# Performance work log

Measured on AMD Instinct MI355X. Metric: run time of the kernel, lower is better.

## Reference

```python
import jax, jax.numpy as jnp
import numpy as np

TOP_K = 4
NORM_TOPK_PROB = True


def setup_inputs() -> dict:
    key = jax.random.key(0)
    kx, kg, k1, k3, k2 = jax.random.split(key, 5)
    B, S, H, I, E = 1, 2048, 1024, 512, 16
    scale = 0.02
    return {
        "hidden_states": jax.random.normal(kx, (B, S, H), jnp.float32),
        "gate_w": jax.random.normal(kg, (E, H), jnp.float32) * scale,   # router Linear weight [E,H]
        "w1": jax.random.normal(k1, (E, I, H), jnp.float32) * scale,    # intermediateDense per expert
        "w3": jax.random.normal(k3, (E, I, H), jnp.float32) * scale,    # intermediateDense2 per expert
        "w2": jax.random.normal(k2, (E, H, I), jnp.float32) * scale,    # outputDense per expert
    }


def reference(hidden_states, gate_w, w1, w3, w2):
    B, S, H = hidden_states.shape
    x = hidden_states.reshape(-1, H)                    # [T,H]
    T = x.shape[0]
    E = gate_w.shape[0]

    # Router: softmax in fp32, top-k, optional renorm (norm_topk_prob=True)
    router_logits = x @ gate_w.T                        # [T,E]
    probs = jax.nn.softmax(router_logits.astype(jnp.float32), axis=-1)
    routing_weights, selected = jax.lax.top_k(probs, TOP_K)   # [T,K], [T,K]
    if NORM_TOPK_PROB:
        routing_weights = routing_weights / routing_weights.sum(-1, keepdims=True)
    routing_weights = routing_weights.astype(x.dtype)

    # Dense per-token expert-weight matrix: zero for unselected experts, so
    # the combine below computes exactly the torch gather->FFN->index_add math.
    w = jnp.zeros((T, E), x.dtype).at[jnp.arange(T)[:, None], selected].add(routing_weights)

    # Gated SiLU FFN for every expert, combined with routing weights.
    h1 = jnp.einsum('th,eih->tei', x, w1)               # [T,E,I]
    h3 = jnp.einsum('th,eih->tei', x, w3)               # [T,E,I]
    act = jax.nn.silu(h1) * h3                          # [T,E,I]
    out = jnp.einsum('tei,ehi,te->th', act, w2, w)      # [T,H]
    return out.reshape(B, S, H)
```

## Files before the change

### kernel.cpp

```cpp
#include <hip/hip_runtime.h>
#include <hip/hip_bf16.h>

#define T 2048
#define H 1024
#define IDIM 512
#define E 16
#define TOPK 4
#define NPAIR (T * TOPK)

typedef short bf16x8 __attribute__((ext_vector_type(8)));
typedef float f32x4 __attribute__((ext_vector_type(4)));

static __device__ __forceinline__ unsigned short f2bf(float f) {
    union { float f; unsigned int u; } v; v.f = f;
    unsigned int r = (v.u + 0x7FFFu + ((v.u >> 16) & 1u)) >> 16;
    return (unsigned short)r;
}
static __device__ __forceinline__ float bf2f(unsigned short s) {
    union { unsigned int u; float f; } v; v.u = ((unsigned int)s) << 16;
    return v.f;
}

static __device__ __forceinline__ void async_ld16(const unsigned short* g, unsigned short* l) {
    __builtin_amdgcn_global_load_lds((const __attribute__((address_space(1))) void*)g,
                                     (__attribute__((address_space(3))) void*)l, 16, 0, 0);
}

__global__ __launch_bounds__(256) void cvt_kernel(
    const float* __restrict__ src, unsigned short* __restrict__ dst, int n4)
{
    int i = blockIdx.x * blockDim.x + threadIdx.x;
    int stride = gridDim.x * blockDim.x;
    for (; i < n4; i += stride) {
        float4 v = ((const float4*)src)[i];
        ushort4 o;
        o.x = f2bf(v.x); o.y = f2bf(v.y); o.z = f2bf(v.z); o.w = f2bf(v.w);
        ((ushort4*)dst)[i] = o;
    }
}

__global__ __launch_bounds__(256) void router_kernel(
    const float* __restrict__ x, const float* __restrict__ gw,
    int* __restrict__ topk_idx, float* __restrict__ topk_w,
    unsigned short* __restrict__ xb)
{
    int tok = blockIdx.x * 4 + (threadIdx.x >> 6);
    int lane = threadIdx.x & 63;
    if (tok >= T) return;
    const float4* xt4 = (const float4*)(x + (size_t)tok * H);
    float4 xr[4];
#pragma unroll
    for (int j = 0; j < 4; ++j) xr[j] = xt4[lane + j * 64];
    ushort4* xbt = (ushort4*)(xb + (size_t)tok * H);
#pragma unroll
    for (int j = 0; j < 4; ++j) {
        ushort4 o;
        o.x = f2bf(xr[j].x); o.y = f2bf(xr[j].y);
        o.z = f2bf(xr[j].z); o.w = f2bf(xr[j].w);
        xbt[lane + j * 64] = o;
    }
    float logits[E];
#pragma unroll
    for (int e = 0; e < E; ++e) {
        const float4* ge4 = (const float4*)(gw + (size_t)e * H);
        float acc = 0.f;
#pragma unroll
        for (int j = 0; j < 4; ++j) {
            float4 g = ge4[lane + j * 64];
            acc += xr[j].x * g.x + xr[j].y * g.y + xr[j].z * g.z + xr[j].w * g.w;
        }
#pragma unroll
        for (int off = 32; off; off >>= 1) acc += __shfl_xor(acc, off, 64);
        logits[e] = acc;
    }
    if (lane == 0) {
        float m = logits[0];
#pragma unroll
        for (int e = 1; e < E; ++e) m = fmaxf(m, logits[e]);
        float p[E];
#pragma unroll
        for (int e = 0; e < E; ++e) p[e] = __expf(logits[e] - m);
        int sel[TOPK]; float wv[TOPK]; float tot = 0.f;
#pragma unroll
        for (int k = 0; k < TOPK; ++k) {
            int best = 0; float bv = -1.f;
#pragma unroll
            for (int e = 0; e < E; ++e) { if (p[e] > bv) { bv = p[e]; best = e; } }
            sel[k] = best; wv[k] = bv; tot += bv; p[best] = -2.f;
        }
#pragma unroll
        for (int k = 0; k < TOPK; ++k) {
            topk_idx[tok * TOPK + k] = sel[k];
            topk_w[tok * TOPK + k] = wv[k] / tot;
        }
    }
}

__global__ __launch_bounds__(256) void hist_kernel(
    const int* __restrict__ topk_idx, int* __restrict__ offsets)
{
    __shared__ int h[4][E];
    int tid = threadIdx.x, wave = tid >> 6;
    if (tid < 4 * E) ((int*)h)[tid] = 0;
    __syncthreads();
    for (int i = tid; i < NPAIR; i += 256) atomicAdd(&h[wave][topk_idx[i]], 1);
    __syncthreads();
    if (tid == 0) {
        int s = 0;
#pragma unroll
        for (int e = 0; e < E; ++e) {
            offsets[e] = s;
            s += h[0][e] + h[1][e] + h[2][e] + h[3][e];
        }
        offsets[E] = s;
    }
}

__global__ __launch_bounds__(256) void scatter_kernel(
    const int* __restrict__ topk_idx,
    const int* __restrict__ offsets, int* __restrict__ cursor,
    int* __restrict__ pair_token, int* __restrict__ inv_pos)
{
    __shared__ int lh[E];
    __shared__ int base[E];
    int tid = threadIdx.x;
    int i = blockIdx.x * 256 + tid;
    if (tid < E) lh[tid] = 0;
    __syncthreads();
    int e = topk_idx[i];
    int lr = atomicAdd(&lh[e], 1);
    __syncthreads();
    if (tid < E) base[tid] = atomicAdd(&cursor[tid], lh[tid]);
    __syncthreads();
    int pos = offsets[e] + base[e] + lr;
    pair_token[pos] = i >> 2;
    inv_pos[i] = pos;
}

__global__ __launch_bounds__(256) void gemm_a_kernel(
    const unsigned short* __restrict__ xb,
    const unsigned short* __restrict__ wb1,
    const unsigned short* __restrict__ wb3,
    const int* __restrict__ offsets,
    const int* __restrict__ pair_token,
    unsigned short* __restrict__ act)
{
    __shared__ unsigned short Xs[2][128 * 64];
    __shared__ unsigned short W1s[2][64 * 64];
    __shared__ unsigned short W3s[2][64 * 64];

    int bid = blockIdx.x;
    int xcd = bid & 7, s = bid >> 3;
    int yz = xcd * 16 + (s >> 4);
    int e = yz >> 3;
    int n0 = (yz & 7) * 64;
    int t0 = (s & 15) * 128;

    int beg = offsets[e];
    int cnt = offsets[e + 1] - beg;
    if (t0 >= cnt) return;

    int tid = threadIdx.x;
    int wave = tid >> 6, lane = tid & 63;
    int lrow8 = lane >> 3;
    int csw = (lane & 7) ^ lrow8;

    const unsigned short* xg[4];
#pragma unroll
    for (int i = 0; i < 4; ++i) {
        int row = wave * 32 + i * 8 + lrow8;
        int r = t0 + row; if (r >= cnt) r = cnt - 1;
        xg[i] = xb + (size_t)pair_token[beg + r] * H + csw * 8;
    }
    const unsigned short* w1g[2];
    const unsigned short* w3g[2];
    size_t wbase = (size_t)e * IDIM * H;
#pragma unroll
    for (int i = 0; i < 2; ++i) {
        int row = wave * 16 + i * 8 + lrow8;
        w1g[i] = wb1 + wbase + (size_t)(n0 + row) * H + csw * 8;
        w3g[i] = wb3 + wbase + (size_t)(n0 + row) * H + csw * 8;
    }

    int wr = wave >> 1, wc = wave & 1;
    int lm = lane & 15, lq = lane >> 4;

    f32x4 acc1[4][2], acc3[4][2];
#pragma unroll
    for (int mi = 0; mi < 4; ++mi)
#pragma unroll
        for (int nj = 0; nj < 2; ++nj) {
            acc1[mi][nj] = (f32x4){0.f, 0.f, 0.f, 0.f};
            acc3[mi][nj] = (f32x4){0.f, 0.f, 0.f, 0.f};
        }

#pragma unroll
    for (int i = 0; i < 4; ++i) async_ld16(xg[i], &Xs[0][(wave * 32 + i * 8) * 64]);
#pragma unroll
    for (int i = 0; i < 2; ++i) {
        async_ld16(w1g[i], &W1s[0][(wave * 16 + i * 8) * 64]);
        async_ld16(w3g[i], &W3s[0][(wave * 16 + i * 8) * 64]);
    }

    const int NK = H / 64;
    for (int kk = 0; kk < NK; ++kk) {
        int cur = kk & 1;
        __syncthreads();
        if (kk + 1 < NK) {
            int nxt = cur ^ 1;
            int k1 = (kk + 1) * 64;
#pragma unroll
            for (int i = 0; i < 4; ++i) async_ld16(xg[i] + k1, &Xs[nxt][(wave * 32 + i * 8) * 64]);
#pragma unroll
            for (int i = 0; i < 2; ++i) {
                async_ld16(w1g[i] + k1, &W1s[nxt][(wave * 16 + i * 8) * 64]);
                async_ld16(w3g[i] + k1, &W3s[nxt][(wave * 16 + i * 8) * 64]);
            }
        }
#pragma unroll
        for (int ks = 0; ks < 2; ++ks) {
            int cc = ks * 4 + lq;
            bf16x8 af[4], b1[2], b3[2];
#pragma unroll
            for (int mi = 0; mi < 4; ++mi) {
                int m = wr * 64 + mi * 16 + lm;
                af[mi] = *(const bf16x8*)&Xs[cur][m * 64 + ((cc ^ (m & 7)) << 3)];
            }
#pragma unroll
            for (int nj = 0; nj < 2; ++nj) {
                int n = wc * 32 + nj * 16 + lm;
                b1[nj] = *(const bf16x8*)&W1s[cur][n * 64 + ((cc ^ (n & 7)) << 3)];
                b3[nj] = *(const bf16x8*)&W3s[cur][n * 64 + ((cc ^ (n & 7)) << 3)];
            }
#pragma unroll
            for (int mi = 0; mi < 4; ++mi)
#pragma unroll
                for (int nj = 0; nj < 2; ++nj) {
                    acc1[mi][nj] = __builtin_amdgcn_mfma_f32_16x16x32_bf16(af[mi], b1[nj], acc1[mi][nj], 0, 0, 0);
                    acc3[mi][nj] = __builtin_amdgcn_mfma_f32_16x16x32_bf16(af[mi], b3[nj], acc3[mi][nj], 0, 0, 0);
                }
        }
    }
#pragma unroll
    for (int mi = 0; mi < 4; ++mi) {
#pragma unroll
        for (int r = 0; r < 4; ++r) {
            int trow = t0 + wr * 64 + mi * 16 + lq * 4 + r;
            if (trow < cnt) {
                size_t base = (size_t)(beg + trow) * IDIM + n0 + wc * 32 + lm;
#pragma unroll
                for (int nj = 0; nj < 2; ++nj) {
                    float h1 = acc1[mi][nj][r];
                    float sg = h1 / (1.f + __expf(-h1));
                    act[base + nj * 16] = f2bf(sg * acc3[mi][nj][r]);
                }
            }
        }
    }
}

__global__ __launch_bounds__(256) void gemm_b_kernel(
    const unsigned short* __restrict__ act,
    const unsigned short* __restrict__ wb2,
    const int* __restrict__ offsets,
    unsigned short* __restrict__ outp)
{
    __shared__ unsigned short As[2][128 * 64];
    __shared__ unsigned short W2s[2][64 * 64];

    int bid = blockIdx.x;
    int xcd = bid & 7, s = bid >> 3;
    int yz = xcd * 32 + (s >> 4);
    int e = yz >> 4;
    int h0 = (yz & 15) * 64;
    int t0 = (s & 15) * 128;

    int beg = offsets[e];
    int cnt = offsets[e + 1] - beg;
    if (t0 >= cnt) return;

    int tid = threadIdx.x;
    int wave = tid >> 6, lane = tid & 63;
    int lrow8 = lane >> 3;
    int csw = (lane & 7) ^ lrow8;

    const unsigned short* ag[4];
#pragma unroll
    for (int i = 0; i < 4; ++i) {
        int row = wave * 32 + i * 8 + lrow8;
        int ar = beg + t0 + row; if (ar > NPAIR - 1) ar = NPAIR - 1;
        ag[i] = act + (size_t)ar * IDIM + csw * 8;
    }
    const unsigned short* w2g[2];
    size_t wbase = (size_t)e * H * IDIM;
#pragma unroll
    for (int i = 0; i < 2; ++i) {
        int row = wave * 16 + i * 8 + lrow8;
        w2g[i] = wb2 + wbase + (size_t)(h0 + row) * IDIM + csw * 8;
    }

    int wr = wave >> 1, wc = wave & 1;
    int lm = lane & 15, lq = lane >> 4;

    f32x4 acc[4][2];
#pragma unroll
    for (int mi = 0; mi < 4; ++mi)
#pragma unroll
        for (int nj = 0; nj < 2; ++nj) acc[mi][nj] = (f32x4){0.f, 0.f, 0.f, 0.f};

#pragma unroll
    for (int i = 0; i < 4; ++i) async_ld16(ag[i], &As[0][(wave * 32 + i * 8) * 64]);
#pragma unroll
    for (int i = 0; i < 2; ++i) async_ld16(w2g[i], &W2s[0][(wave * 16 + i * 8) * 64]);

    const int NK = IDIM / 64;
    for (int kk = 0; kk < NK; ++kk) {
        int cur = kk & 1;
        __syncthreads();
        if (kk + 1 < NK) {
            int nxt = cur ^ 1;
            int k1 = (kk + 1) * 64;
#pragma unroll
            for (int i = 0; i < 4; ++i) async_ld16(ag[i] + k1, &As[nxt][(wave * 32 + i * 8) * 64]);
#pragma unroll
            for (int i = 0; i < 2; ++i) async_ld16(w2g[i] + k1, &W2s[nxt][(wave * 16 + i * 8) * 64]);
        }
#pragma unroll
        for (int ks = 0; ks < 2; ++ks) {
            int cc = ks * 4 + lq;
            bf16x8 af[4], bfr[2];
#pragma unroll
            for (int mi = 0; mi < 4; ++mi) {
                int m = wr * 64 + mi * 16 + lm;
                af[mi] = *(const bf16x8*)&As[cur][m * 64 + ((cc ^ (m & 7)) << 3)];
            }
#pragma unroll
            for (int nj = 0; nj < 2; ++nj) {
                int n = wc * 32 + nj * 16 + lm;
                bfr[nj] = *(const bf16x8*)&W2s[cur][n * 64 + ((cc ^ (n & 7)) << 3)];
            }
#pragma unroll
            for (int mi = 0; mi < 4; ++mi)
#pragma unroll
                for (int nj = 0; nj < 2; ++nj)
                    acc[mi][nj] = __builtin_amdgcn_mfma_f32_16x16x32_bf16(af[mi], bfr[nj], acc[mi][nj], 0, 0, 0);
        }
    }
#pragma unroll
    for (int mi = 0; mi < 4; ++mi) {
#pragma unroll
        for (int r = 0; r < 4; ++r) {
            int trow = t0 + wr * 64 + mi * 16 + lq * 4 + r;
            if (trow < cnt) {
                unsigned short* orow = outp + (size_t)(beg + trow) * H + h0 + wc * 32 + lm;
#pragma unroll
                for (int nj = 0; nj < 2; ++nj) orow[nj * 16] = f2bf(acc[mi][nj][r]);
            }
        }
    }
}

__global__ __launch_bounds__(256) void combine_kernel(
    const unsigned short* __restrict__ outp, const int* __restrict__ inv_pos,
    const float* __restrict__ topk_w, float* __restrict__ out)
{
    int gid = blockIdx.x * 256 + threadIdx.x;
    int t = gid >> 8;
    int c4 = gid & 255;
    float4 a = make_float4(0.f, 0.f, 0.f, 0.f);
#pragma unroll
    for (int k = 0; k < TOPK; ++k) {
        int pos = inv_pos[t * TOPK + k];
        float w = topk_w[t * TOPK + k];
        ushort4 v = ((const ushort4*)(outp + (size_t)pos * H))[c4];
        a.x += w * bf2f(v.x); a.y += w * bf2f(v.y);
        a.z += w * bf2f(v.z); a.w += w * bf2f(v.w);
    }
    *(float4*)(out + (size_t)t * H + c4 * 4) = a;
}

extern "C" void kernel_launch(void* const* d_in, const int* in_sizes, int n_in,
                              void* d_out, int out_size, void* d_ws, size_t ws_size,
                              hipStream_t stream)
{
    const float* x  = (const float*)d_in[0];
    const float* gw = (const float*)d_in[1];
    const float* w1 = (const float*)d_in[2];
    const float* w3 = (const float*)d_in[3];
    const float* w2 = (const float*)d_in[4];
    float* out = (float*)d_out;

    char* ws = (char*)d_ws;
    int*   cursor     = (int*)(ws + 64);
    int*   offsets    = (int*)(ws + 128);
    int*   topk_idx   = (int*)(ws + 1024);
    float* topk_w     = (float*)(ws + 33792);
    int*   pair_token = (int*)(ws + 66560);
    int*   inv_pos    = (int*)(ws + 99328);
    unsigned short* xb  = (unsigned short*)(ws + 262144);
    unsigned short* wb1 = (unsigned short*)(ws + 8388608);
    unsigned short* wb3 = (unsigned short*)(ws + 25165824);
    unsigned short* wb2 = (unsigned short*)(ws + 41943040);
    unsigned short* act = (unsigned short*)(ws + 58720256);
    unsigned short* outp = (unsigned short*)(ws + 8388608);

    hipMemsetAsync(ws, 0, 256, stream);

    router_kernel<<<T / 4, 256, 0, stream>>>(x, gw, topk_idx, topk_w, xb);
    hist_kernel<<<1, 256, 0, stream>>>(topk_idx, offsets);
    scatter_kernel<<<NPAIR / 256, 256, 0, stream>>>(topk_idx, offsets, cursor,
                                                    pair_token, inv_pos);

    cvt_kernel<<<2048, 256, 0, stream>>>(w1, wb1, (E * IDIM * H) / 4);
    cvt_kernel<<<2048, 256, 0, stream>>>(w3, wb3, (E * IDIM * H) / 4);
    cvt_kernel<<<2048, 256, 0, stream>>>(w2, wb2, (E * H * IDIM) / 4);

    gemm_a_kernel<<<2048, 256, 0, stream>>>(xb, wb1, wb3, offsets, pair_token, act);
    gemm_b_kernel<<<4096, 256, 0, stream>>>(act, wb2, offsets, outp);
    combine_kernel<<<(T * H / 4) / 256, 256, 0, stream>>>(outp, inv_pos, topk_w, out);
}
```

Measured before the change: 234.4 us.

## Halve GEMM K-tile to 32 for occupancy and fuse weight conversion kernels

Both expert GEMMs now stage K-tiles of 32 instead of 64, with a new swizzled LDS layout that packs two rows per 64-element group. This halves shared memory per block, and launch bounds request 5 blocks per CU, so more blocks can be resident to hide latency. The cost is twice as many barriers per GEMM. The three fp32-to-bf16 weight conversions are also merged into a single launch to cut launch overhead.

```diff
diff --git a/kernel.cpp b/kernel.cpp
--- a/kernel.cpp
+++ b/kernel.cpp
@@ -26,11 +26,18 @@
                                      (__attribute__((address_space(3))) void*)l, 16, 0, 0);
 }
 
-__global__ __launch_bounds__(256) void cvt_kernel(
-    const float* __restrict__ src, unsigned short* __restrict__ dst, int n4)
-{
-    int i = blockIdx.x * blockDim.x + threadIdx.x;
-    int stride = gridDim.x * blockDim.x;
+__global__ __launch_bounds__(256) void cvt3_kernel(
+    const float* __restrict__ w1, const float* __restrict__ w3, const float* __restrict__ w2,
+    unsigned short* __restrict__ d1, unsigned short* __restrict__ d3, unsigned short* __restrict__ d2)
+{
+    const int n4 = (E * IDIM * H) / 4;
+    int region = blockIdx.x >> 11;
+    int bid = blockIdx.x & 2047;
+    const float* src = (region == 0) ? w1 : (region == 1) ? w3 : w2;
+    unsigned short* dst = (region == 0) ? d1 : (region == 1) ? d3 : d2;
+    int i = bid * 256 + threadIdx.x;
+    const int stride = 2048 * 256;
+#pragma unroll 4
     for (; i < n4; i += stride) {
         float4 v = ((const float4*)src)[i];
         ushort4 o;
@@ -137,7 +144,8 @@
     inv_pos[i] = pos;
 }
 
-__global__ __launch_bounds__(256) void gemm_a_kernel(
+
+__global__ __launch_bounds__(256, 5) void gemm_a_kernel(
     const unsigned short* __restrict__ xb,
     const unsigned short* __restrict__ wb1,
     const unsigned short* __restrict__ wb3,
@@ -145,16 +153,16 @@
     const int* __restrict__ pair_token,
     unsigned short* __restrict__ act)
 {
-    __shared__ unsigned short Xs[2][128 * 64];
-    __shared__ unsigned short W1s[2][64 * 64];
-    __shared__ unsigned short W3s[2][64 * 64];
+    __shared__ unsigned short Xs[2][128 * 32];
+    __shared__ unsigned short W1s[2][64 * 32];
+    __shared__ unsigned short W3s[2][64 * 32];
 
     int bid = blockIdx.x;
-    int xcd = bid & 7, s = bid >> 3;
-    int yz = xcd * 16 + (s >> 4);
+    int xcd = bid & 7, s0 = bid >> 3;
+    int yz = xcd * 16 + (s0 >> 4);
     int e = yz >> 3;
     int n0 = (yz & 7) * 64;
-    int t0 = (s & 15) * 128;
+    int t0 = (s0 & 15) * 128;
 
     int beg = offsets[e];
     int cnt = offsets[e + 1] - beg;
@@ -162,24 +170,25 @@
 
     int tid = threadIdx.x;
     int wave = tid >> 6, lane = tid & 63;
-    int lrow8 = lane >> 3;
-    int csw = (lane & 7) ^ lrow8;
-
-    const unsigned short* xg[4];
-#pragma unroll
-    for (int i = 0; i < 4; ++i) {
-        int row = wave * 32 + i * 8 + lrow8;
+
+    const unsigned short* xg[2];
+#pragma unroll
+    for (int i = 0; i < 2; ++i) {
+        int slot = wave * 128 + i * 64 + lane;
+        int g = slot >> 3, sp = (slot & 7) ^ (g & 7);
+        int row = g * 2 + (sp >> 2), c = sp & 3;
         int r = t0 + row; if (r >= cnt) r = cnt - 1;
-        xg[i] = xb + (size_t)pair_token[beg + r] * H + csw * 8;
-    }
-    const unsigned short* w1g[2];
-    const unsigned short* w3g[2];
-    size_t wbase = (size_t)e * IDIM * H;
-#pragma unroll
-    for (int i = 0; i < 2; ++i) {
-        int row = wave * 16 + i * 8 + lrow8;
-        w1g[i] = wb1 + wbase + (size_t)(n0 + row) * H + csw * 8;
-        w3g[i] = wb3 + wbase + (size_t)(n0 + row) * H + csw * 8;
+        xg[i] = xb + (size_t)pair_token[beg + r] * H + c * 8;
+    }
+    const unsigned short* w1g;
+    const unsigned short* w3g;
+    {
+        int slot = wave * 64 + lane;
+        int g = slot >> 3, sp = (slot & 7) ^ (g & 7);
+        int row = g * 2 + (sp >> 2), c = sp & 3;
+        size_t off = (size_t)e * IDIM * H + (size_t)(n0 + row) * H + c * 8;
+        w1g = wb1 + off;
+        w3g = wb3 + off;
     }
 
     int wr = wave >> 1, wc = wave & 1;
@@ -194,52 +203,52 @@
             acc3[mi][nj] = (f32x4){0.f, 0.f, 0.f, 0.f};
         }
 
-#pragma unroll
-    for (int i = 0; i < 4; ++i) async_ld16(xg[i], &Xs[0][(wave * 32 + i * 8) * 64]);
-#pragma unroll
-    for (int i = 0; i < 2; ++i) {
-        async_ld16(w1g[i], &W1s[0][(wave * 16 + i * 8) * 64]);
-        async_ld16(w3g[i], &W3s[0][(wave * 16 + i * 8) * 64]);
-    }
-
-    const int NK = H / 64;
+    int aoff[4], boff[2];
+#pragma unroll
+    for (int mi = 0; mi < 4; ++mi) {
+        int m = wr * 64 + mi * 16 + lm;
+        int g = m >> 1;
+        aoff[mi] = g * 64 + (((lq + ((m & 1) << 2)) ^ (g & 7)) << 3);
+    }
+#pragma unroll
+    for (int nj = 0; nj < 2; ++nj) {
+        int n = wc * 32 + nj * 16 + lm;
+        int g = n >> 1;
+        boff[nj] = g * 64 + (((lq + ((n & 1) << 2)) ^ (g & 7)) << 3);
+    }
+
+#pragma unroll
+    for (int i = 0; i < 2; ++i) async_ld16(xg[i], &Xs[0][(wave * 128 + i * 64) * 8]);
+    async_ld16(w1g, &W1s[0][wave * 512]);
+    async_ld16(w3g, &W3s[0][wave * 512]);
+
+    const int NK = H / 32;
     for (int kk = 0; kk < NK; ++kk) {
         int cur = kk & 1;
         __syncthreads();
         if (kk + 1 < NK) {
             int nxt = cur ^ 1;
-            int k1 = (kk + 1) * 64;
-#pragma unroll
-            for (int i = 0; i < 4; ++i) async_ld16(xg[i] + k1, &Xs[nxt][(wave * 32 + i * 8) * 64]);
-#pragma unroll
-            for (int i = 0; i < 2; ++i) {
-                async_ld16(w1g[i] + k1, &W1s[nxt][(wave * 16 + i * 8) * 64]);
-                async_ld16(w3g[i] + k1, &W3s[nxt][(wave * 16 + i * 8) * 64]);
+            int k1 = (kk + 1) * 32;
+#pragma unroll
+            for (int i = 0; i < 2; ++i) async_ld16(xg[i] + k1, &Xs[nxt][(wave * 128 + i * 64) * 8]);
+            async_ld16(w1g + k1, &W1s[nxt][wave * 512]);
+            async_ld16(w3g + k1, &W3s[nxt][wave * 512]);
+        }
+        bf16x8 af[4], b1[2], b3[2];
+#pragma unroll
+        for (int mi = 0; mi < 4; ++mi) af[mi] = *(const bf16x8*)&Xs[cur][aoff[mi]];
+#pragma unroll
+        for (int nj = 0; nj < 2; ++nj) {
+            b1[nj] = *(const bf16x8*)&W1s[cur][boff[nj]];
+            b3[nj] = *(const bf16x8*)&W3s[cur][boff[nj]];
+        }
+#pragma unroll
+        for (int mi = 0; mi < 4; ++mi)
+#pragma unroll
+            for (int nj = 0; nj < 2; ++nj) {
+                acc1[mi][nj] = __builtin_amdgcn_mfma_f32_16x16x32_bf16(af[mi], b1[nj], acc1[mi][nj], 0, 0, 0);
+                acc3[mi][nj] = __builtin_amdgcn_mfma_f32_16x16x32_bf16(af[mi], b3[nj], acc3[mi][nj], 0, 0, 0);
             }
-        }
-#pragma unroll
-        for (int ks = 0; ks < 2; ++ks) {
-            int cc = ks * 4 + lq;
-            bf16x8 af[4], b1[2], b3[2];
-#pragma unroll
-            for (int mi = 0; mi < 4; ++mi) {
-                int m = wr * 64 + mi * 16 + lm;
-                af[mi] = *(const bf16x8*)&Xs[cur][m * 64 + ((cc ^ (m & 7)) << 3)];
-            }
-#pragma unroll
-            for (int nj = 0; nj < 2; ++nj) {
-                int n = wc * 32 + nj * 16 + lm;
-                b1[nj] = *(const bf16x8*)&W1s[cur][n * 64 + ((cc ^ (n & 7)) << 3)];
-                b3[nj] = *(const bf16x8*)&W3s[cur][n * 64 + ((cc ^ (n & 7)) << 3)];
-            }
-#pragma unroll
-            for (int mi = 0; mi < 4; ++mi)
-#pragma unroll
-                for (int nj = 0; nj < 2; ++nj) {
-                    acc1[mi][nj] = __builtin_amdgcn_mfma_f32_16x16x32_bf16(af[mi], b1[nj], acc1[mi][nj], 0, 0, 0);
-                    acc3[mi][nj] = __builtin_amdgcn_mfma_f32_16x16x32_bf16(af[mi], b3[nj], acc3[mi][nj], 0, 0, 0);
-                }
-        }
     }
 #pragma unroll
     for (int mi = 0; mi < 4; ++mi) {
@@ -259,21 +268,21 @@
     }
 }
 
-__global__ __launch_bounds__(256) void gemm_b_kernel(
+__global__ __launch_bounds__(256, 5) void gemm_b_kernel(
     const unsigned short* __restrict__ act,
     const unsigned short* __restrict__ wb2,
     const int* __restrict__ offsets,
     unsigned short* __restrict__ outp)
 {
-    __shared__ unsigned short As[2][128 * 64];
-    __shared__ unsigned short W2s[2][64 * 64];
+    __shared__ unsigned short As[2][128 * 32];
+    __shared__ unsigned short W2s[2][64 * 32];
 
     int bid = blockIdx.x;
-    int xcd = bid & 7, s = bid >> 3;
-    int yz = xcd * 32 + (s >> 4);
+    int xcd = bid & 7, s0 = bid >> 3;
+    int yz = xcd * 32 + (s0 >> 4);
     int e = yz >> 4;
     int h0 = (yz & 15) * 64;
-    int t0 = (s & 15) * 128;
+    int t0 = (s0 & 15) * 128;
 
     int beg = offsets[e];
     int cnt = offsets[e + 1] - beg;
@@ -281,22 +290,22 @@
 
     int tid = threadIdx.x;
     int wave = tid >> 6, lane = tid & 63;
-    int lrow8 = lane >> 3;
-    int csw = (lane & 7) ^ lrow8;
-
-    const unsigned short* ag[4];
-#pragma unroll
-    for (int i = 0; i < 4; ++i) {
-        int row = wave * 32 + i * 8 + lrow8;
+
+    const unsigned short* ag[2];
+#pragma unroll
+    for (int i = 0; i < 2; ++i) {
+        int slot = wave * 128 + i * 64 + lane;
+        int g = slot >> 3, sp = (slot & 7) ^ (g & 7);
+        int row = g * 2 + (sp >> 2), c = sp & 3;
         int ar = beg + t0 + row; if (ar > NPAIR - 1) ar = NPAIR - 1;
-        ag[i] = act + (size_t)ar * IDIM + csw * 8;
-    }
-    const unsigned short* w2g[2];
-    size_t wbase = (size_t)e * H * IDIM;
-#pragma unroll
-    for (int i = 0; i < 2; ++i) {
-        int row = wave * 16 + i * 8 + lrow8;
-        w2g[i] = wb2 + wbase + (size_t)(h0 + row) * IDIM + csw * 8;
+        ag[i] = act + (size_t)ar * IDIM + c * 8;
+    }
+    const unsigned short* w2g;
+    {
+        int slot = wave * 64 + lane;
+        int g = slot >> 3, sp = (slot & 7) ^ (g & 7);
+        int row = g * 2 + (sp >> 2), c = sp & 3;
+        w2g = wb2 + (size_t)e * H * IDIM + (size_t)(h0 + row) * IDIM + c * 8;
     }
 
     int wr = wave >> 1, wc = wave & 1;
@@ -308,43 +317,45 @@
 #pragma unroll
         for (int nj = 0; nj < 2; ++nj) acc[mi][nj] = (f32x4){0.f, 0.f, 0.f, 0.f};
 
-#pragma unroll
-    for (int i = 0; i < 4; ++i) async_ld16(ag[i], &As[0][(wave * 32 + i * 8) * 64]);
-#pragma unroll
-    for (int i = 0; i < 2; ++i) async_ld16(w2g[i], &W2s[0][(wave * 16 + i * 8) * 64]);
-
-    const int NK = IDIM / 64;
+    int aoff[4], boff[2];
+#pragma unroll
+    for (int mi = 0; mi < 4; ++mi) {
+        int m = wr * 64 + mi * 16 + lm;
+        int g = m >> 1;
+        aoff[mi] = g * 64 + (((lq + ((m & 1) << 2)) ^ (g & 7)) << 3);
+    }
+#pragma unroll
+    for (int nj = 0; nj < 2; ++nj) {
+        int n = wc * 32 + nj * 16 + lm;
+        int g = n >> 1;
+        boff[nj] = g * 64 + (((lq + ((n & 1) << 2)) ^ (g & 7)) << 3);
+    }
+
+#pragma unroll
+    for (int i = 0; i < 2; ++i) async_ld16(ag[i], &As[0][(wave * 128 + i * 64) * 8]);
+    async_ld16(w2g, &W2s[0][wave * 512]);
+
+    const int NK = IDIM / 32;
     for (int kk = 0; kk < NK; ++kk) {
         int cur = kk & 1;
         __syncthreads();
         if (kk + 1 < NK) {
             int nxt = cur ^ 1;
-            int k1 = (kk + 1) * 64;
-#pragma unroll
-            for (int i = 0; i < 4; ++i) async_ld16(ag[i] + k1, &As[nxt][(wave * 32 + i * 8) * 64]);
-#pragma unroll
-            for (int i = 0; i < 2; ++i) async_ld16(w2g[i] + k1, &W2s[nxt][(wave * 16 + i * 8) * 64]);
-        }
-#pragma unroll
-        for (int ks = 0; ks < 2; ++ks) {
-            int cc = ks * 4 + lq;
-            bf16x8 af[4], bfr[2];
-#pragma unroll
-            for (int mi = 0; mi < 4; ++mi) {
-                int m = wr * 64 + mi * 16 + lm;
-                af[mi] = *(const bf16x8*)&As[cur][m * 64 + ((cc ^ (m & 7)) << 3)];
-            }
-#pragma unroll
-            for (int nj = 0; nj < 2; ++nj) {
-                int n = wc * 32 + nj * 16 + lm;
-                bfr[nj] = *(const bf16x8*)&W2s[cur][n * 64 + ((cc ^ (n & 7)) << 3)];
-            }
-#pragma unroll
-            for (int mi = 0; mi < 4; ++mi)
-#pragma unroll
-                for (int nj = 0; nj < 2; ++nj)
-                    acc[mi][nj] = __builtin_amdgcn_mfma_f32_16x16x32_bf16(af[mi], bfr[nj], acc[mi][nj], 0, 0, 0);
-        }
+            int k1 = (kk + 1) * 32;
+#pragma unroll
+            for (int i = 0; i < 2; ++i) async_ld16(ag[i] + k1, &As[nxt][(wave * 128 + i * 64) * 8]);
+            async_ld16(w2g + k1, &W2s[nxt][wave * 512]);
+        }
+        bf16x8 af[4], bfr[2];
+#pragma unroll
+        for (int mi = 0; mi < 4; ++mi) af[mi] = *(const bf16x8*)&As[cur][aoff[mi]];
+#pragma unroll
+        for (int nj = 0; nj < 2; ++nj) bfr[nj] = *(const bf16x8*)&W2s[cur][boff[nj]];
+#pragma unroll
+        for (int mi = 0; mi < 4; ++mi)
+#pragma unroll
+            for (int nj = 0; nj < 2; ++nj)
+                acc[mi][nj] = __builtin_amdgcn_mfma_f32_16x16x32_bf16(af[mi], bfr[nj], acc[mi][nj], 0, 0, 0);
     }
 #pragma unroll
     for (int mi = 0; mi < 4; ++mi) {
@@ -411,9 +422,7 @@
     scatter_kernel<<<NPAIR / 256, 256, 0, stream>>>(topk_idx, offsets, cursor,
                                                     pair_token, inv_pos);
 
-    cvt_kernel<<<2048, 256, 0, stream>>>(w1, wb1, (E * IDIM * H) / 4);
-    cvt_kernel<<<2048, 256, 0, stream>>>(w3, wb3, (E * IDIM * H) / 4);
-    cvt_kernel<<<2048, 256, 0, stream>>>(w2, wb2, (E * H * IDIM) / 4);
+    cvt3_kernel<<<3 * 2048, 256, 0, stream>>>(w1, w3, w2, wb1, wb3, wb2);
 
     gemm_a_kernel<<<2048, 256, 0, stream>>>(xb, wb1, wb3, offsets, pair_token, act);
     gemm_b_kernel<<<4096, 256, 0, stream>>>(act, wb2, offsets, outp);
```

Result: faster. 229.3 us (-2.2%).
